# Kernel tuning notes

Measured on AMD Instinct MI355X. Metric: run time of the kernel, lower is better.

The kernel has to match this reference:

```python
import jax, jax.numpy as jnp
import numpy as np

N, IN_DIM, OUT_DIM, H = 8192, 128, 128, 2
HD = OUT_DIM // H
NEG_SLOPE = 0.2


def setup_inputs() -> dict:
    key = jax.random.key(0)
    k1, k2, k3, k4, k5 = jax.random.split(key, 5)
    x = jax.random.normal(k1, (N, IN_DIM), dtype=jnp.float32)
    adj = jax.random.randint(k2, (N, N), 0, 2).astype(jnp.float32)
    W = jax.random.normal(k3, (IN_DIM, OUT_DIM), dtype=jnp.float32) / np.sqrt(IN_DIM)
    a_src = jax.random.normal(k4, (H, HD), dtype=jnp.float32) * 0.01
    a_dst = jax.random.normal(k5, (H, HD), dtype=jnp.float32) * 0.01
    return {"x": x, "adj": adj, "W": W, "a_src": a_src, "a_dst": a_dst}


def reference(x, adj, W, a_src, a_dst):
    # h: (N, H, HD)
    h = (x @ W).reshape(N, H, HD)
    # per-node additive score halves: (N, H)
    e_src = jnp.einsum('nhd,hd->nh', h, a_src)
    e_dst = jnp.einsum('nhd,hd->nh', h, a_dst)
    # attn logits: (N_i, N_j, H); torch code adds e_src[i] + e_dst[j]
    logits = jax.nn.leaky_relu(e_src[:, None, :] + e_dst[None, :, :], NEG_SLOPE)
    logits = jnp.where(adj[:, :, None] > 0, logits, -jnp.inf)
    # softmax over neighbor axis j (dim=1), matching F.softmax(attn, dim=1)
    attn = jax.nn.softmax(logits, axis=1)
    # dropout omitted (eval mode)
    out = jnp.einsum('ijh,jhd->ihd', attn, h).reshape(N, OUT_DIM)
    return out
```

## Files before the change

### kernel.cpp

```cpp
#include <hip/hip_runtime.h>
#include <hip/hip_bf16.h>

#define N 8192
#define IND 128
#define OUTD 128
#define JC 8
#define JLEN 1024
#define STEPS 32

typedef float f32x4 __attribute__((ext_vector_type(4)));
typedef short s16x8 __attribute__((ext_vector_type(8)));
typedef _Float16 f16;
typedef _Float16 f16x4 __attribute__((ext_vector_type(4)));

static __device__ inline unsigned short f2bf(float f) {
    union { float f; unsigned u; } v; v.f = f;
    unsigned u = v.u + 0x7fffu + ((v.u >> 16) & 1u);
    return (unsigned short)(u >> 16);
}
static __device__ inline float bf2f(unsigned short b) {
    union { unsigned u; float f; } v; v.u = ((unsigned)b) << 16;
    return v.f;
}

__global__ __launch_bounds__(256) void k1_xw(const float* __restrict__ x,
                                             const float* __restrict__ W,
                                             unsigned short* __restrict__ hT) {
    __shared__ unsigned short Wl[128 * 130];
    const int tid = threadIdx.x;
    {
        int k = tid >> 1, n0 = (tid & 1) * 64;
        const float4* src = (const float4*)(W + k * 128 + n0);
#pragma unroll
        for (int v = 0; v < 16; ++v) {
            float4 f = src[v];
            int base = k * 130 + n0 + v * 4;
            Wl[base + 0] = f2bf(f.x);
            Wl[base + 1] = f2bf(f.y);
            Wl[base + 2] = f2bf(f.z);
            Wl[base + 3] = f2bf(f.w);
        }
    }
    __syncthreads();
    const int wave = tid >> 6, lane = tid & 63;
    const int m = lane & 15, quad = lane >> 4;
    const int ibase = blockIdx.x * 64 + wave * 16;
    const int irow = ibase + m;

    f32x4 acc[8];
#pragma unroll
    for (int t = 0; t < 8; ++t) acc[t] = (f32x4){0.f, 0.f, 0.f, 0.f};

#pragma unroll
    for (int ks = 0; ks < 4; ++ks) {
        const int k0 = ks * 32 + quad * 8;
        const float4* xp = (const float4*)(x + (size_t)irow * 128 + k0);
        float4 xa = xp[0], xb = xp[1];
        s16x8 afrag;
        afrag[0] = (short)f2bf(xa.x); afrag[1] = (short)f2bf(xa.y);
        afrag[2] = (short)f2bf(xa.z); afrag[3] = (short)f2bf(xa.w);
        afrag[4] = (short)f2bf(xb.x); afrag[5] = (short)f2bf(xb.y);
        afrag[6] = (short)f2bf(xb.z); afrag[7] = (short)f2bf(xb.w);
#pragma unroll
        for (int nt = 0; nt < 8; ++nt) {
            const int n = nt * 16 + m;
            s16x8 bfrag;
#pragma unroll
            for (int j = 0; j < 8; ++j)
                bfrag[j] = (short)Wl[(k0 + j) * 130 + n];
            acc[nt] = __builtin_amdgcn_mfma_f32_16x16x32_bf16(afrag, bfrag, acc[nt], 0, 0, 0);
        }
    }
#pragma unroll
    for (int nt = 0; nt < 8; ++nt) {
        const int c = nt * 16 + m;
        const int i0 = ibase + quad * 4;
        ushort4 pk;
        pk.x = f2bf(acc[nt][0]); pk.y = f2bf(acc[nt][1]);
        pk.z = f2bf(acc[nt][2]); pk.w = f2bf(acc[nt][3]);
        *(ushort4*)(hT + (size_t)c * N + i0) = pk;
    }
}

__global__ __launch_bounds__(256) void k2_e(const unsigned short* __restrict__ hT,
                                            const float* __restrict__ a_src,
                                            const float* __restrict__ a_dst,
                                            float* __restrict__ As, float* __restrict__ Cs,
                                            float4* __restrict__ BD) {
    const int i = blockIdx.x * 256 + threadIdx.x;
    float es0 = 0.f, ed0 = 0.f, es1 = 0.f, ed1 = 0.f;
#pragma unroll 8
    for (int c = 0; c < 128; ++c) {
        float v = bf2f(hT[(size_t)c * N + i]);
        float as = a_src[c], ad = a_dst[c];
        if (c < 64) { es0 += v * as; ed0 += v * ad; }
        else        { es1 += v * as; ed1 += v * ad; }
    }
    As[i]     = __expf(es0);
    As[N + i] = __expf(es1);
    Cs[i]     = __expf(0.2f * es0);
    Cs[N + i] = __expf(0.2f * es1);
    float4 bd;
    bd.x = __expf(ed0); bd.y = __expf(0.2f * ed0);
    bd.z = __expf(ed1); bd.w = __expf(0.2f * ed1);
    BD[i] = bd;
}

__global__ __launch_bounds__(256, 3) void k3_main(const float* __restrict__ adj,
                                                  const unsigned short* __restrict__ hT,
                                                  const float* __restrict__ As,
                                                  const float* __restrict__ Cs,
                                                  const float4* __restrict__ BD,
                                                  f16* __restrict__ Up,
                                                  float* __restrict__ Lp) {
    __shared__ float4 BDl[JLEN + JLEN / 8];
    const int tid = threadIdx.x;
    const int wave = tid >> 6, lane = tid & 63;
    const int m = lane & 15, quad = lane >> 4;
    const int ibase = blockIdx.x * 64 + wave * 16;
    const int irow = ibase + m;
    const int jc = blockIdx.y;
    const int j0 = jc * JLEN;

    for (int t = tid; t < JLEN; t += 256) BDl[t + (t >> 3)] = BD[j0 + t];

    const float A0 = As[irow], C0 = Cs[irow];
    const float A1 = As[N + irow], C1 = Cs[N + irow];

    f32x4 acc[2][4];
#pragma unroll
    for (int h = 0; h < 2; ++h)
#pragma unroll
        for (int nt = 0; nt < 4; ++nt) acc[h][nt] = (f32x4){0.f, 0.f, 0.f, 0.f};
    float ls0 = 0.f, ls1 = 0.f;

    const float* adjrow = adj + (size_t)irow * N;
    __syncthreads();

    float4 aja = *(const float4*)(adjrow + j0 + quad * 8);
    float4 ajb = *(const float4*)(adjrow + j0 + quad * 8 + 4);

#pragma unroll 1
    for (int s = 0; s < STEPS; ++s) {
        const int jq = j0 + s * 32 + quad * 8;

        s16x8 h0[4], h1[4];
#pragma unroll
        for (int nt = 0; nt < 4; ++nt) {
            h0[nt] = *(const s16x8*)(hT + (size_t)(nt * 16 + m) * N + jq);
            h1[nt] = *(const s16x8*)(hT + (size_t)(nt * 16 + m + 64) * N + jq);
        }

        const int sn = (s + 1) & (STEPS - 1);
        const int jqn = j0 + sn * 32 + quad * 8;
        float4 ana = *(const float4*)(adjrow + jqn);
        float4 anb = *(const float4*)(adjrow + jqn + 4);

        const int bbase = s * 32 + quad * 8;
        const int bidx = bbase + (bbase >> 3);
        float ajv[8];
        *(float4*)(ajv)     = aja;
        *(float4*)(ajv + 4) = ajb;
        s16x8 p0, p1;
#pragma unroll
        for (int jj = 0; jj < 8; ++jj) {
            float4 bd = BDl[bidx + jj];
            float w0 = fmaxf(A0 * bd.x, C0 * bd.y);
            float pv0 = ajv[jj] * w0;
            ls0 += pv0;
            p0[jj] = (short)f2bf(pv0);
            float w1 = fmaxf(A1 * bd.z, C1 * bd.w);
            float pv1 = ajv[jj] * w1;
            ls1 += pv1;
            p1[jj] = (short)f2bf(pv1);
        }

#pragma unroll
        for (int nt = 0; nt < 4; ++nt) {
            acc[0][nt] = __builtin_amdgcn_mfma_f32_16x16x32_bf16(p0, h0[nt], acc[0][nt], 0, 0, 0);
            acc[1][nt] = __builtin_amdgcn_mfma_f32_16x16x32_bf16(p1, h1[nt], acc[1][nt], 0, 0, 0);
        }
        aja = ana; ajb = anb;
    }

    ls0 += __shfl_xor(ls0, 16, 64);
    ls0 += __shfl_xor(ls0, 32, 64);
    ls1 += __shfl_xor(ls1, 16, 64);
    ls1 += __shfl_xor(ls1, 32, 64);

    f16* Ub = Up + (size_t)jc * N * 128;
#pragma unroll
    for (int h = 0; h < 2; ++h)
#pragma unroll
        for (int nt = 0; nt < 4; ++nt) {
            const int c = h * 64 + nt * 16 + m;
            const int ib = ibase + quad * 4;
#pragma unroll
            for (int r = 0; r < 4; ++r)
                Ub[(size_t)(ib + r) * 128 + c] = (f16)acc[h][nt][r];
        }
    if (quad == 0) {
        Lp[((size_t)jc * 2 + 0) * N + irow] = ls0;
        Lp[((size_t)jc * 2 + 1) * N + irow] = ls1;
    }
}

__global__ __launch_bounds__(256) void k4_reduce(const f16* __restrict__ Up,
                                                 const float* __restrict__ Lp,
                                                 float* __restrict__ out) {
    const int base = (blockIdx.x * 256 + threadIdx.x) * 4;
    const int i = base >> 7, c = base & 127, h = c >> 6;
    float su0 = 0.f, su1 = 0.f, su2 = 0.f, su3 = 0.f, sl = 0.f;
#pragma unroll
    for (int jcc = 0; jcc < JC; ++jcc) {
        f16x4 u = *(const f16x4*)(Up + (size_t)jcc * N * 128 + base);
        su0 += (float)u[0]; su1 += (float)u[1];
        su2 += (float)u[2]; su3 += (float)u[3];
        sl += Lp[((size_t)jcc * 2 + h) * N + i];
    }
    float inv = 1.0f / sl;
    float4 o; o.x = su0 * inv; o.y = su1 * inv; o.z = su2 * inv; o.w = su3 * inv;
    *(float4*)(out + base) = o;
}

extern "C" void kernel_launch(void* const* d_in, const int* in_sizes, int n_in,
                              void* d_out, int out_size, void* d_ws, size_t ws_size,
                              hipStream_t stream) {
    const float* x     = (const float*)d_in[0];
    const float* adj   = (const float*)d_in[1];
    const float* W     = (const float*)d_in[2];
    const float* a_src = (const float*)d_in[3];
    const float* a_dst = (const float*)d_in[4];
    float* out = (float*)d_out;
    char* ws = (char*)d_ws;

    size_t off = 0;
    unsigned short* hT = (unsigned short*)(ws + off); off += (size_t)128 * N * 2;
    float* As = (float*)(ws + off); off += (size_t)2 * N * 4;
    float* Cs = (float*)(ws + off); off += (size_t)2 * N * 4;
    float4* BD = (float4*)(ws + off); off += (size_t)N * 16;

    f16* Up = (f16*)(ws + off);
    float* Lp = (float*)(ws + off + (size_t)JC * N * 128 * 2);

    k1_xw<<<N / 64, 256, 0, stream>>>(x, W, hT);
    k2_e<<<N / 256, 256, 0, stream>>>(hT, a_src, a_dst, As, Cs, BD);
    dim3 g3(N / 64, JC);
    k3_main<<<g3, 256, 0, stream>>>(adj, hT, As, Cs, BD, Up, Lp);
    k4_reduce<<<(N * 128) / (256 * 4), 256, 0, stream>>>(Up, Lp, out);
}
```

Baseline: 538.9 us.

## Stage adj and hT tiles into LDS via async double-buffered global_load_lds

The main attention kernel no longer has each wave load its own hT fragments and adjacency rows from global memory. The block now issues asynchronous global-to-LDS copies into double-buffered shared tiles, with a swizzle so the hT tile is fetched once per block and shared by all four waves. The BD table is loaded the same way. The aim is to remove the four-fold redundant hT global traffic and to hide load latency behind the MFMA work, at the cost of a block-wide barrier every step and more LDS use, which may lower occupancy.

```diff
diff --git a/kernel.cpp b/kernel.cpp
--- a/kernel.cpp
+++ b/kernel.cpp
@@ -21,6 +21,12 @@
 static __device__ inline float bf2f(unsigned short b) {
     union { unsigned u; float f; } v; v.u = ((unsigned)b) << 16;
     return v.f;
+}
+
+static __device__ __forceinline__ void async16(const void* g, void* l) {
+    __builtin_amdgcn_global_load_lds(
+        (const __attribute__((address_space(1))) unsigned int*)g,
+        (__attribute__((address_space(3))) unsigned int*)l, 16, 0, 0);
 }
 
 __global__ __launch_bounds__(256) void k1_xw(const float* __restrict__ x,
@@ -113,7 +119,10 @@
                                                   const float4* __restrict__ BD,
                                                   f16* __restrict__ Up,
                                                   float* __restrict__ Lp) {
-    __shared__ float4 BDl[JLEN + JLEN / 8];
+    __shared__ float4 BDl[JLEN];
+    __shared__ float4 adjbuf[2][4][2][64];
+    __shared__ float4 hbuf[2][8][64];
+
     const int tid = threadIdx.x;
     const int wave = tid >> 6, lane = tid & 63;
     const int m = lane & 15, quad = lane >> 4;
@@ -122,8 +131,6 @@
     const int jc = blockIdx.y;
     const int j0 = jc * JLEN;
 
-    for (int t = tid; t < JLEN; t += 256) BDl[t + (t >> 3)] = BD[j0 + t];
-
     const float A0 = As[irow], C0 = Cs[irow];
     const float A1 = As[N + irow], C1 = Cs[N + irow];
 
@@ -135,36 +142,61 @@
     float ls0 = 0.f, ls1 = 0.f;
 
     const float* adjrow = adj + (size_t)irow * N;
+    const size_t adjsrow = (size_t)(ibase + (lane & 15)) * N;
+
+    const int hr = lane >> 2;
+    const int hcs = ((lane & 3) - ((hr >> 1) & 3)) & 3;
+
+#pragma unroll
+    for (int c = 0; c < 4; ++c)
+        async16(BD + j0 + (wave * 4 + c) * 64 + lane, &BDl[(wave * 4 + c) * 64]);
+    {
+        const int jb = j0;
+        async16(adj + adjsrow + jb + (lane >> 4) * 8,     &adjbuf[0][wave][0][0]);
+        async16(adj + adjsrow + jb + (lane >> 4) * 8 + 4, &adjbuf[0][wave][1][0]);
+#pragma unroll
+        for (int cc = 0; cc < 2; ++cc) {
+            const int g = wave * 2 + cc;
+            async16(hT + (size_t)(g * 16 + hr) * N + jb + hcs * 8, &hbuf[0][g][0]);
+        }
+    }
     __syncthreads();
 
-    float4 aja = *(const float4*)(adjrow + j0 + quad * 8);
-    float4 ajb = *(const float4*)(adjrow + j0 + quad * 8 + 4);
+    const int slotp = (quad + ((m >> 1) & 3)) & 3;
 
 #pragma unroll 1
     for (int s = 0; s < STEPS; ++s) {
-        const int jq = j0 + s * 32 + quad * 8;
-
-        s16x8 h0[4], h1[4];
-#pragma unroll
-        for (int nt = 0; nt < 4; ++nt) {
-            h0[nt] = *(const s16x8*)(hT + (size_t)(nt * 16 + m) * N + jq);
-            h1[nt] = *(const s16x8*)(hT + (size_t)(nt * 16 + m + 64) * N + jq);
-        }
-
-        const int sn = (s + 1) & (STEPS - 1);
-        const int jqn = j0 + sn * 32 + quad * 8;
-        float4 ana = *(const float4*)(adjrow + jqn);
-        float4 anb = *(const float4*)(adjrow + jqn + 4);
-
-        const int bbase = s * 32 + quad * 8;
-        const int bidx = bbase + (bbase >> 3);
+        const int p = s & 1;
+        if (s + 1 < STEPS) {
+            const int pb = p ^ 1;
+            const int jb = j0 + (s + 1) * 32;
+            async16(adj + adjsrow + jb + (lane >> 4) * 8,     &adjbuf[pb][wave][0][0]);
+            async16(adj + adjsrow + jb + (lane >> 4) * 8 + 4, &adjbuf[pb][wave][1][0]);
+#pragma unroll
+            for (int cc = 0; cc < 2; ++cc) {
+                const int g = wave * 2 + cc;
+                async16(hT + (size_t)(g * 16 + hr) * N + jb + hcs * 8, &hbuf[pb][g][0]);
+            }
+        }
+
+        float4 aja = adjbuf[p][wave][0][lane];
+        float4 ajb = adjbuf[p][wave][1][lane];
         float ajv[8];
         *(float4*)(ajv)     = aja;
         *(float4*)(ajv + 4) = ajb;
+
+        s16x8 h0[4], h1[4];
+#pragma unroll
+        for (int nt = 0; nt < 4; ++nt) {
+            h0[nt] = *(const s16x8*)&hbuf[p][nt][m * 4 + slotp];
+            h1[nt] = *(const s16x8*)&hbuf[p][4 + nt][m * 4 + slotp];
+        }
+
         s16x8 p0, p1;
+        const int bb = s * 32 + quad * 8;
 #pragma unroll
         for (int jj = 0; jj < 8; ++jj) {
-            float4 bd = BDl[bidx + jj];
+            float4 bd = BDl[bb + jj];
             float w0 = fmaxf(A0 * bd.x, C0 * bd.y);
             float pv0 = ajv[jj] * w0;
             ls0 += pv0;
@@ -180,7 +212,8 @@
             acc[0][nt] = __builtin_amdgcn_mfma_f32_16x16x32_bf16(p0, h0[nt], acc[0][nt], 0, 0, 0);
             acc[1][nt] = __builtin_amdgcn_mfma_f32_16x16x32_bf16(p1, h1[nt], acc[1][nt], 0, 0, 0);
         }
-        aja = ana; ajb = anb;
+
+        __syncthreads();
     }
 
     ls0 += __shfl_xor(ls0, 16, 64);
@@ -203,6 +236,7 @@
         Lp[((size_t)jc * 2 + 0) * N + irow] = ls0;
         Lp[((size_t)jc * 2 + 1) * N + irow] = ls1;
     }
+    (void)adjrow;
 }
 
 __global__ __launch_bounds__(256) void k4_reduce(const f16* __restrict__ Up,
```

After: 455.8 us. 15.4% less time.

## Deepen adjacency prefetch, fully unroll j-loop, and swap grid axes in main kernel

Applied to the files above, without the earlier changes.

Restructures the main attention kernel's j-loop. It now double-buffers 128 columns of adjacency per outer step instead of one 32-column step ahead, and the loop is fully unrolled so the compiler can schedule more loads ahead of use. It also swaps the grid dimensions so consecutive blocks take different j-chunks of the same row group, which changes L2 locality for the adj rows and hT. Occupancy is lowered to 2 blocks per SIMD to fit the larger register footprint, which may reduce latency hiding across waves.

```diff
diff --git a/kernel.cpp b/kernel.cpp
--- a/kernel.cpp
+++ b/kernel.cpp
@@ -6,7 +6,7 @@
 #define OUTD 128
 #define JC 8
 #define JLEN 1024
-#define STEPS 32
+#define OSTEPS 8
 
 typedef float f32x4 __attribute__((ext_vector_type(4)));
 typedef short s16x8 __attribute__((ext_vector_type(8)));
@@ -106,7 +106,7 @@
     BD[i] = bd;
 }
 
-__global__ __launch_bounds__(256, 3) void k3_main(const float* __restrict__ adj,
+__global__ __launch_bounds__(256, 2) void k3_main(const float* __restrict__ adj,
                                                   const unsigned short* __restrict__ hT,
                                                   const float* __restrict__ As,
                                                   const float* __restrict__ Cs,
@@ -117,9 +117,9 @@
     const int tid = threadIdx.x;
     const int wave = tid >> 6, lane = tid & 63;
     const int m = lane & 15, quad = lane >> 4;
-    const int ibase = blockIdx.x * 64 + wave * 16;
+    const int ibase = blockIdx.y * 64 + wave * 16;
     const int irow = ibase + m;
-    const int jc = blockIdx.y;
+    const int jc = blockIdx.x;
     const int j0 = jc * JLEN;
 
     for (int t = tid; t < JLEN; t += 256) BDl[t + (t >> 3)] = BD[j0 + t];
@@ -134,53 +134,58 @@
         for (int nt = 0; nt < 4; ++nt) acc[h][nt] = (f32x4){0.f, 0.f, 0.f, 0.f};
     float ls0 = 0.f, ls1 = 0.f;
 
-    const float* adjrow = adj + (size_t)irow * N;
+    const float* adjrow = adj + (size_t)irow * N + j0;
     __syncthreads();
 
-    float4 aja = *(const float4*)(adjrow + j0 + quad * 8);
-    float4 ajb = *(const float4*)(adjrow + j0 + quad * 8 + 4);
-
-#pragma unroll 1
-    for (int s = 0; s < STEPS; ++s) {
-        const int jq = j0 + s * 32 + quad * 8;
-
-        s16x8 h0[4], h1[4];
-#pragma unroll
-        for (int nt = 0; nt < 4; ++nt) {
-            h0[nt] = *(const s16x8*)(hT + (size_t)(nt * 16 + m) * N + jq);
-            h1[nt] = *(const s16x8*)(hT + (size_t)(nt * 16 + m + 64) * N + jq);
-        }
-
-        const int sn = (s + 1) & (STEPS - 1);
-        const int jqn = j0 + sn * 32 + quad * 8;
-        float4 ana = *(const float4*)(adjrow + jqn);
-        float4 anb = *(const float4*)(adjrow + jqn + 4);
-
-        const int bbase = s * 32 + quad * 8;
-        const int bidx = bbase + (bbase >> 3);
-        float ajv[8];
-        *(float4*)(ajv)     = aja;
-        *(float4*)(ajv + 4) = ajb;
-        s16x8 p0, p1;
-#pragma unroll
-        for (int jj = 0; jj < 8; ++jj) {
-            float4 bd = BDl[bidx + jj];
-            float w0 = fmaxf(A0 * bd.x, C0 * bd.y);
-            float pv0 = ajv[jj] * w0;
-            ls0 += pv0;
-            p0[jj] = (short)f2bf(pv0);
-            float w1 = fmaxf(A1 * bd.z, C1 * bd.w);
-            float pv1 = ajv[jj] * w1;
-            ls1 += pv1;
-            p1[jj] = (short)f2bf(pv1);
-        }
-
-#pragma unroll
-        for (int nt = 0; nt < 4; ++nt) {
-            acc[0][nt] = __builtin_amdgcn_mfma_f32_16x16x32_bf16(p0, h0[nt], acc[0][nt], 0, 0, 0);
-            acc[1][nt] = __builtin_amdgcn_mfma_f32_16x16x32_bf16(p1, h1[nt], acc[1][nt], 0, 0, 0);
-        }
-        aja = ana; ajb = anb;
+    float4 aj[2][8];
+#pragma unroll
+    for (int kc = 0; kc < 4; ++kc) {
+        aj[0][kc * 2]     = *(const float4*)(adjrow + kc * 32 + quad * 8);
+        aj[0][kc * 2 + 1] = *(const float4*)(adjrow + kc * 32 + quad * 8 + 4);
+    }
+
+#pragma unroll
+    for (int os = 0; os < OSTEPS; ++os) {
+        const int cur = os & 1, nxt = cur ^ 1;
+        const int osn = (os < OSTEPS - 1) ? os + 1 : os;
+#pragma unroll
+        for (int kc = 0; kc < 4; ++kc) {
+            aj[nxt][kc * 2]     = *(const float4*)(adjrow + osn * 128 + kc * 32 + quad * 8);
+            aj[nxt][kc * 2 + 1] = *(const float4*)(adjrow + osn * 128 + kc * 32 + quad * 8 + 4);
+        }
+#pragma unroll
+        for (int kc = 0; kc < 4; ++kc) {
+            const int jq = j0 + os * 128 + kc * 32 + quad * 8;
+            s16x8 h0[4], h1[4];
+#pragma unroll
+            for (int nt = 0; nt < 4; ++nt) {
+                h0[nt] = *(const s16x8*)(hT + (size_t)(nt * 16 + m) * N + jq);
+                h1[nt] = *(const s16x8*)(hT + (size_t)(nt * 16 + m + 64) * N + jq);
+            }
+            float ajv[8];
+            *(float4*)(ajv)     = aj[cur][kc * 2];
+            *(float4*)(ajv + 4) = aj[cur][kc * 2 + 1];
+            const int bb = os * 128 + kc * 32 + quad * 8;
+            const int bidx = bb + (bb >> 3);
+            s16x8 p0, p1;
+#pragma unroll
+            for (int jj = 0; jj < 8; ++jj) {
+                float4 bd = BDl[bidx + jj];
+                float w0 = fmaxf(A0 * bd.x, C0 * bd.y);
+                float pv0 = ajv[jj] * w0;
+                ls0 += pv0;
+                p0[jj] = (short)f2bf(pv0);
+                float w1 = fmaxf(A1 * bd.z, C1 * bd.w);
+                float pv1 = ajv[jj] * w1;
+                ls1 += pv1;
+                p1[jj] = (short)f2bf(pv1);
+            }
+#pragma unroll
+            for (int nt = 0; nt < 4; ++nt) {
+                acc[0][nt] = __builtin_amdgcn_mfma_f32_16x16x32_bf16(p0, h0[nt], acc[0][nt], 0, 0, 0);
+                acc[1][nt] = __builtin_amdgcn_mfma_f32_16x16x32_bf16(p1, h1[nt], acc[1][nt], 0, 0, 0);
+            }
+        }
     }
 
     ls0 += __shfl_xor(ls0, 16, 64);
@@ -245,7 +250,7 @@
 
     k1_xw<<<N / 64, 256, 0, stream>>>(x, W, hT);
     k2_e<<<N / 256, 256, 0, stream>>>(hT, a_src, a_dst, As, Cs, BD);
-    dim3 g3(N / 64, JC);
+    dim3 g3(JC, N / 64);
     k3_main<<<g3, 256, 0, stream>>>(adj, hT, As, Cs, BD, Up, Lp);
     k4_reduce<<<(N * 128) / (256 * 4), 256, 0, stream>>>(Up, Lp, out);
 }
```

New measurement: 511.2 us. -5.1%, faster.
